# Kernel tuning notes

Measured on AMD Instinct MI355X. Metric: run time of the kernel, lower is better.

## Reference

```python
import jax, jax.numpy as jnp
import numpy as np

NCLASSES = 21
CONF_THRESH = 0.5
IOU_THRESH = 0.45
TOP_K = 200
NMS_MAX_OUT = 400
NEG = jnp.float32(-1e9)  # sentinel for suppressed / below-threshold scores

B, N_BOXES = 8, 8732
LAST = NCLASSES + 4 * (NCLASSES - 1) + 1  # 102


def setup_inputs() -> dict:
    key = jax.random.key(0)
    kc, kxy, kwh, ke = jax.random.split(key, 4)
    conf = jax.random.uniform(kc, (B, N_BOXES, NCLASSES), dtype=jnp.float32)
    # plausible normalized boxes: xmin,ymin in [0,0.8], width/height in [0.01,0.2]
    xy = jax.random.uniform(kxy, (B, N_BOXES, NCLASSES - 1, 2), minval=0.0, maxval=0.8)
    wh = jax.random.uniform(kwh, (B, N_BOXES, NCLASSES - 1, 2), minval=0.01, maxval=0.2)
    boxes = jnp.concatenate([xy, xy + wh], axis=-1).reshape(B, N_BOXES, 4 * (NCLASSES - 1))
    extra = jax.random.uniform(ke, (B, N_BOXES, 1), dtype=jnp.float32)
    y_pred = jnp.concatenate([conf, boxes, extra], axis=-1)  # [B, N, 102]
    return {"y_pred": y_pred}


def _iou_one_vs_all(box, boxes):
    # box: [4] (xmin,ymin,xmax,ymax); boxes: [N,4]
    x1 = jnp.maximum(box[0], boxes[:, 0])
    y1 = jnp.maximum(box[1], boxes[:, 1])
    x2 = jnp.minimum(box[2], boxes[:, 2])
    y2 = jnp.minimum(box[3], boxes[:, 3])
    inter = jnp.maximum(x2 - x1, 0.0) * jnp.maximum(y2 - y1, 0.0)
    area_a = (box[2] - box[0]) * (box[3] - box[1])
    area_b = (boxes[:, 2] - boxes[:, 0]) * (boxes[:, 3] - boxes[:, 1])
    union = area_a + area_b - inter
    return jnp.where(union > 0.0, inter / union, 0.0)


def _nms_one_class(rows):
    # rows: [N, 7] = (class_id, conf, xmin, ymin, xmax, ymax, extra)
    n = rows.shape[0]
    scores0 = jnp.where(rows[:, 1] > CONF_THRESH, rows[:, 1], NEG)
    boxes = rows[:, 2:6]
    idx_range = jnp.arange(n)

    def step(live, _):
        best = jnp.argmax(live)
        valid = live[best] > NEG * 0.5  # any real score passed the threshold
        ious = _iou_one_vs_all(boxes[best], boxes)
        suppress = valid & ((ious > IOU_THRESH) | (idx_range == best))
        live = jnp.where(suppress, NEG, live)
        return live, (best, valid)

    _, (sel, selv) = jax.lax.scan(step, scores0, None, length=NMS_MAX_OUT)
    # gather selected rows; zero-pad invalid slots (matches tf.pad with 0)
    out = jnp.where(selv[:, None], rows[sel], 0.0)  # [NMS_MAX_OUT, 7]
    return out


def _per_image(item):
    # item: [N, 102]
    n = item.shape[0]
    conf = item[:, 1:NCLASSES]                                  # [N, C-1]
    boxes = item[:, NCLASSES:NCLASSES + 4 * (NCLASSES - 1)].reshape(n, NCLASSES - 1, 4)
    extra = item[:, -1]                                         # [N]
    class_ids = jnp.arange(1, NCLASSES, dtype=item.dtype)       # [C-1]
    rows = jnp.concatenate([
        jnp.broadcast_to(class_ids[:, None, None], (NCLASSES - 1, n, 1)),
        conf.T[:, :, None],
        jnp.transpose(boxes, (1, 0, 2)),
        jnp.broadcast_to(extra[None, :, None], (NCLASSES - 1, n, 1)),
    ], axis=-1)                                                 # [C-1, N, 7]
    per_class = jax.vmap(_nms_one_class)(rows)                  # [C-1, MAX_OUT, 7]
    filtered = per_class.reshape(-1, 7)                         # [(C-1)*MAX_OUT, 7]
    _, top_idx = jax.lax.top_k(filtered[:, 1], TOP_K)           # sorted descending
    return filtered[top_idx]                                    # [TOP_K, 7]


def reference(y_pred):
    return jax.vmap(_per_image)(y_pred)  # [B, TOP_K, 7]
```

## Files before the change

### kernel.cpp

```cpp
#include <hip/hip_runtime.h>
#include <cstdint>

#define NB 8
#define NBOX 8732
#define NCL 21
#define NCM1 20
#define LASTD 102
#define CONF_TH 0.5f
#define IOU_TH 0.45f
#define TOPK 200
#define MAXOUT 400
#define SELCAP 200
#define EMITN 256
#define NTASK (NB * NCM1)
#define THREADS 1024
#define NW 16
#define NIT 9
#define NBIN 2048
#define KPAD 8768
#define NBATCH (KPAD / 64)

#define MIDD ((double)IOU_TH + 0x1p-26)

struct SM {
    float4 selbox[SELCAP];
    float selA[SELCAP];
    uint64_t selkey[SELCAP];
    uint64_t keys[KPAD];
    uint64_t smask[2][64];
    unsigned long long supW[2][NW];
    int hist[NBIN];
    int binstart[NBIN];
    int wavetot[NW];
    int Mshare, nselshare, prevNshare, doneflag;
};

__device__ __forceinline__ int iou_sup(float4 a, float aA, float4 b, float bA) {
    float x1 = fmaxf(a.x, b.x), y1 = fmaxf(a.y, b.y);
    float x2 = fminf(a.z, b.z), y2 = fminf(a.w, b.w);
    float iw = fmaxf(__fsub_rn(x2, x1), 0.0f);
    float ih = fmaxf(__fsub_rn(y2, y1), 0.0f);
    float inter = __fmul_rn(iw, ih);
    float uni = __fsub_rn(__fadd_rn(aA, bA), inter);
    return (double)inter > MIDD * (double)uni;
}

__device__ __forceinline__ float4 load_box(const float* __restrict__ img,
                                           int boxoff, uint64_t key) {
    if ((key >> 32) == 0) return make_float4(0.f, 0.f, 0.f, 0.f);
    uint32_t i = 0xFFFFFFFFu - (uint32_t)key;
    const float* bp = img + (size_t)i * LASTD + boxoff;
    return make_float4(bp[0], bp[1], bp[2], bp[3]);
}

__device__ __forceinline__ float box_area(float4 b) {
    return __fmul_rn(__fsub_rn(b.z, b.x), __fsub_rn(b.w, b.y));
}

__global__ __launch_bounds__(THREADS) void nms_per_class(const float* __restrict__ yp,
                                                         float* __restrict__ rows) {
    __shared__ SM sm;
    const int task = blockIdx.x;
    const int b = task / NCM1;
    const int cm1 = task % NCM1;
    const int tid = threadIdx.x;
    const int lane = tid & 63;
    const int wav = tid >> 6;
    const float* img = yp + (size_t)b * NBOX * LASTD;
    const int boxoff = NCL + 4 * cm1;

    float confs[NIT];
    #pragma unroll
    for (int it = 0; it < NIT; ++it) {
        int idx = it * THREADS + tid;
        confs[it] = (idx < NBOX) ? img[(size_t)idx * LASTD + (1 + cm1)] : 0.0f;
    }
    sm.hist[tid] = 0; sm.hist[tid + THREADS] = 0;
    __syncthreads();

    #pragma unroll
    for (int it = 0; it < NIT; ++it) {
        int idx = it * THREADS + tid;
        if (idx < NBOX && confs[it] > CONF_TH) {
            int bin = (int)((__float_as_uint(confs[it]) - 0x3F000000u) >> 12);
            atomicAdd(&sm.hist[bin], 1);
        }
    }
    __syncthreads();

    int h0 = sm.hist[2 * tid], h1 = sm.hist[2 * tid + 1];
    int x = h0 + h1;
    int s = x;
    #pragma unroll
    for (int d = 1; d <= 32; d <<= 1) {
        int y = __shfl_down(s, d);
        if (lane + d < 64) s += y;
    }
    if (lane == 0) sm.wavetot[wav] = s;
    __syncthreads();
    int cross = 0;
    #pragma unroll
    for (int w = 0; w < NW; ++w)
        if (w > wav) cross += sm.wavetot[w];
    int Safter = cross + s - x;
    sm.binstart[2 * tid + 1] = Safter;
    sm.binstart[2 * tid] = Safter + h1;
    if (tid == 0) sm.Mshare = cross + s;
    sm.hist[2 * tid] = 0; sm.hist[2 * tid + 1] = 0;
    __syncthreads();

    #pragma unroll
    for (int it = 0; it < NIT; ++it) {
        int idx = it * THREADS + tid;
        if (idx < NBOX && confs[it] > CONF_TH) {
            uint32_t bits = __float_as_uint(confs[it]);
            int bin = (int)((bits - 0x3F000000u) >> 12);
            int slot = sm.binstart[bin] + atomicAdd(&sm.hist[bin], 1);
            sm.keys[slot] = ((uint64_t)bits << 32) |
                            (uint32_t)(0xFFFFFFFFu - (uint32_t)idx);
        }
    }
    __syncthreads();
    const int M = sm.Mshare;
    for (int m = M + tid; m < KPAD; m += THREADS) sm.keys[m] = 0;
    for (int f = tid; f < NBIN; f += THREADS) {
        int s0 = sm.binstart[f], h = sm.hist[f];
        for (int i2 = 1; i2 < h; ++i2) {
            uint64_t key = sm.keys[s0 + i2];
            int j = i2 - 1;
            while (j >= 0 && sm.keys[s0 + j] < key) {
                sm.keys[s0 + j + 1] = sm.keys[s0 + j];
                --j;
            }
            sm.keys[s0 + j + 1] = key;
        }
    }
    __syncthreads();

    uint64_t keyC = sm.keys[lane];
    uint64_t keyN = sm.keys[64 + lane];
    float4 boxC = load_box(img, boxoff, keyC);
    float4 boxN = load_box(img, boxoff, keyN);
    float aC = box_area(boxC), aN = box_area(boxN);
    #pragma unroll
    for (int tt = 0; tt < 4; ++tt) {
        int c = wav + tt * NW;
        float4 cb;
        cb.x = __shfl(boxC.x, c); cb.y = __shfl(boxC.y, c);
        cb.z = __shfl(boxC.z, c); cb.w = __shfl(boxC.w, c);
        float ca = __shfl(aC, c);
        uint64_t row = 0;
        if (ca > 0.0f)
            row = __ballot(lane < c && iou_sup(cb, ca, boxC, aC));
        if (lane == 0) sm.smask[0][c] = row;
    }
    if (tid < 2 * NW) ((unsigned long long*)sm.supW)[tid] = 0ull;
    __syncthreads();

    int nsel = 0, prevN = 0;
    bool done = false;
    for (int i = 0; i < NBATCH && !done; ++i) {
        const int p = i & 1;
        const bool vC = (keyC >> 32) != 0;
        {
            int sup = 0;
            for (int j = prevN + wav; j < nsel; j += NW)
                sup |= iou_sup(boxC, aC, sm.selbox[j], sm.selA[j]);
            unsigned long long bal = __ballot(vC && sup);
            if (lane == 0 && bal) atomicOr(&sm.supW[p][wav], bal);
        }
        int f0 = (i + 2) * 64;
        uint64_t key2 = (f0 < KPAD) ? sm.keys[f0 + lane] : 0;
        float4 box2 = load_box(img, boxoff, key2);
        float a2 = box_area(box2);
        __syncthreads();
        const int nselPre = nsel;
        if (wav == 0) {
            unsigned long long V = __ballot(vC);
            unsigned long long E = (lane < NW) ? sm.supW[p][lane] : 0ull;
            #pragma unroll
            for (int d = 1; d < NW; d <<= 1) E |= __shfl_xor(E, d);
            E = __shfl(E, 0);
            if (lane < NW) sm.supW[p][lane] = 0ull;
            uint64_t smc = sm.smask[p][lane];
            uint64_t alive = ~(E | ~V);
            uint64_t accm = 0;
            int cnt = nsel;
            while (alive && cnt < SELCAP) {
                int t = __ffsll((unsigned long long)alive) - 1;
                uint64_t bit = 1ull << t;
                accm |= bit;
                cnt++;
                unsigned long long kill = __ballot((smc >> t) & 1ull);
                alive &= ~(kill | bit);
            }
            if ((accm >> lane) & 1ull) {
                int pos = nsel + __popcll(accm & ((1ull << lane) - 1ull));
                sm.selbox[pos] = boxC;
                sm.selA[pos] = aC;
                sm.selkey[pos] = keyC;
            }
            if (lane == 0) {
                sm.nselshare = cnt;
                sm.prevNshare = nsel;
                sm.doneflag = (cnt >= SELCAP) || (V != ~0ull);
            }
        } else {
            float4 cb[5];
            float ca[5];
            unsigned amask = 0;
            #pragma unroll
            for (int k = 0; k < 5; ++k) {
                int c = (wav - 1) + k * (NW - 1);
                float4 t4 = make_float4(0.f, 0.f, 0.f, 0.f);
                float tA = 0.0f;
                if (c < 64) {
                    t4.x = __shfl(boxN.x, c); t4.y = __shfl(boxN.y, c);
                    t4.z = __shfl(boxN.z, c); t4.w = __shfl(boxN.w, c);
                    tA = __shfl(aN, c);
                }
                cb[k] = t4; ca[k] = tA;
                if (c < 64 && tA > 0.0f) amask |= 1u << k;
            }
            unsigned long long sb = 0;
            for (int j0 = 0; j0 < nselPre && amask; j0 += 64) {
                int j = j0 + lane;
                bool jv = j < nselPre;
                float4 sbx = sm.selbox[jv ? j : 0];
                float sA = sm.selA[jv ? j : 0];
                #pragma unroll
                for (int k = 0; k < 5; ++k) {
                    if (!((amask >> k) & 1u)) continue;
                    int hit = jv && iou_sup(cb[k], ca[k], sbx, sA);
                    if (__ballot(hit)) {
                        amask &= ~(1u << k);
                        sb |= 1ull << ((wav - 1) + k * (NW - 1));
                    }
                }
            }
            #pragma unroll
            for (int k = 0; k < 5; ++k) {
                if (!((amask >> k) & 1u)) continue;
                int c = (wav - 1) + k * (NW - 1);
                uint64_t row = __ballot(lane < c && iou_sup(cb[k], ca[k], boxN, aN));
                if (lane == 0) sm.smask[p ^ 1][c] = row;
            }
            if (lane == 0) sm.supW[p ^ 1][wav] = sb;
        }
        __syncthreads();
        nsel = sm.nselshare;
        prevN = sm.prevNshare;
        done = sm.doneflag != 0;
        keyC = keyN; boxC = boxN; aC = aN;
        keyN = key2; boxN = box2; aN = a2;
    }

    float* out0 = rows + (size_t)task * MAXOUT * 7;
    for (int r = tid; r < EMITN; r += THREADS) {
        float* o = out0 + (size_t)r * 7;
        if (r < nsel) {
            uint64_t key = sm.selkey[r];
            uint32_t i = 0xFFFFFFFFu - (uint32_t)key;
            float4 bx = sm.selbox[r];
            o[0] = (float)(cm1 + 1);
            o[1] = __uint_as_float((uint32_t)(key >> 32));
            o[2] = bx.x;
            o[3] = bx.y;
            o[4] = bx.z;
            o[5] = bx.w;
            o[6] = img[(size_t)i * LASTD + (LASTD - 1)];
        } else {
            #pragma unroll
            for (int q = 0; q < 7; ++q) o[q] = 0.0f;
        }
    }
}

__global__ __launch_bounds__(THREADS) void topk_per_image(const float* __restrict__ rows,
                                                          float* __restrict__ out) {
    __shared__ uint64_t K[8192];
    const int b = blockIdx.x;
    const int tid = threadIdx.x;
    const float* rb = rows + (size_t)b * (NCM1 * MAXOUT) * 7;

    for (int xx = tid; xx < 8192; xx += THREADS) {
        int list = xx >> 8, r = xx & 255;
        uint64_t k = 0;
        if (list < NCM1) {
            int flat = list * MAXOUT + r;
            float conf = rb[(size_t)flat * 7 + 1];
            k = ((uint64_t)__float_as_uint(conf) << 32) |
                (uint32_t)(0xFFFFFFFFu - (uint32_t)flat);
        }
        K[xx] = k;
    }
    __syncthreads();

    for (int round = 0; round < 5; ++round) {
        int npairs = 16 >> round;
        int sep = 256 << round;
        for (int w = tid; w < npairs * 256; w += THREADS) {
            int p = w >> 8, t = w & 255;
            int A = p * 2 * sep;
            uint64_t a = K[A + t];
            uint64_t c = K[A + sep + 255 - t];
            K[A + t] = a > c ? a : c;
        }
        __syncthreads();
        for (int j = 128; j >= 1; j >>= 1) {
            for (int w = tid; w < npairs * 128; w += THREADS) {
                int p = w >> 7, q = w & 127;
                int t = ((q & ~(j - 1)) << 1) | (q & (j - 1));
                int A = p * 2 * sep;
                uint64_t x0 = K[A + t];
                uint64_t x1 = K[A + t + j];
                if (x0 < x1) { K[A + t] = x1; K[A + t + j] = x0; }
            }
            __syncthreads();
        }
    }

    if (tid < TOPK) {
        uint64_t key = K[tid];
        uint32_t flat = 0xFFFFFFFFu - (uint32_t)key;
        const float* src = rb + (size_t)flat * 7;
        float* o = out + ((size_t)b * TOPK + tid) * 7;
        #pragma unroll
        for (int q = 0; q < 7; ++q) o[q] = src[q];
    }
}

extern "C" void kernel_launch(void* const* d_in, const int* in_sizes, int n_in,
                              void* d_out, int out_size, void* d_ws, size_t ws_size,
                              hipStream_t stream) {
    const float* yp = (const float*)d_in[0];
    float* rows = (float*)d_ws;
    float* out = (float*)d_out;

    hipLaunchKernelGGL(nms_per_class, dim3(NTASK), dim3(THREADS), 0, stream, yp, rows);
    hipLaunchKernelGGL(topk_per_image, dim3(NB), dim3(THREADS), 0, stream, rows, out);
}
```

Measured before the change: 67.57 us.

## Split per-class NMS into key-building and greedy-scan kernels via global workspace

```diff
diff --git a/kernel.cpp b/kernel.cpp
--- a/kernel.cpp
+++ b/kernel.cpp
@@ -57,18 +57,15 @@
     return __fmul_rn(__fsub_rn(b.z, b.x), __fsub_rn(b.w, b.y));
 }
 
-__global__ __launch_bounds__(THREADS) void nms_per_class(const float* __restrict__ yp,
-                                                         float* __restrict__ rows) {
-    __shared__ SM sm;
-    const int task = blockIdx.x;
-    const int b = task / NCM1;
-    const int cm1 = task % NCM1;
-    const int tid = threadIdx.x;
-    const int lane = tid & 63;
-    const int wav = tid >> 6;
-    const float* img = yp + (size_t)b * NBOX * LASTD;
-    const int boxoff = NCL + 4 * cm1;
-
+__device__ __forceinline__ float4 shfl_box(float4 b, int c) {
+    float4 r;
+    r.x = __shfl(b.x, c); r.y = __shfl(b.y, c);
+    r.z = __shfl(b.z, c); r.w = __shfl(b.w, c);
+    return r;
+}
+
+__device__ void build_keys(const float* __restrict__ img, int cm1, SM& sm,
+                           int tid, int lane, int wav) {
     float confs[NIT];
     #pragma unroll
     for (int it = 0; it < NIT; ++it) {
@@ -136,7 +133,10 @@
         }
     }
     __syncthreads();
-
+}
+
+__device__ int greedy_scan(const float* __restrict__ img, int boxoff, SM& sm,
+                           int tid, int lane, int wav) {
     uint64_t keyC = sm.keys[lane];
     uint64_t keyN = sm.keys[64 + lane];
     float4 boxC = load_box(img, boxoff, keyC);
@@ -145,9 +145,7 @@
     #pragma unroll
     for (int tt = 0; tt < 4; ++tt) {
         int c = wav + tt * NW;
-        float4 cb;
-        cb.x = __shfl(boxC.x, c); cb.y = __shfl(boxC.y, c);
-        cb.z = __shfl(boxC.z, c); cb.w = __shfl(boxC.w, c);
+        float4 cb = shfl_box(boxC, c);
         float ca = __shfl(aC, c);
         uint64_t row = 0;
         if (ca > 0.0f)
@@ -215,8 +213,7 @@
                 float4 t4 = make_float4(0.f, 0.f, 0.f, 0.f);
                 float tA = 0.0f;
                 if (c < 64) {
-                    t4.x = __shfl(boxN.x, c); t4.y = __shfl(boxN.y, c);
-                    t4.z = __shfl(boxN.z, c); t4.w = __shfl(boxN.w, c);
+                    t4 = shfl_box(boxN, c);
                     tA = __shfl(aN, c);
                 }
                 cb[k] = t4; ca[k] = tA;
@@ -254,7 +251,12 @@
         keyC = keyN; boxC = boxN; aC = aN;
         keyN = key2; boxN = box2; aN = a2;
     }
-
+    return nsel;
+}
+
+__device__ void emit_rows(const float* __restrict__ img, int cm1, SM& sm,
+                          int nsel, float* __restrict__ rows, int task,
+                          int tid) {
     float* out0 = rows + (size_t)task * MAXOUT * 7;
     for (int r = tid; r < EMITN; r += THREADS) {
         float* o = out0 + (size_t)r * 7;
@@ -276,6 +278,48 @@
     }
 }
 
+__global__ __launch_bounds__(THREADS) void nms_front(const float* __restrict__ yp,
+                                                     uint64_t* __restrict__ keysG) {
+    __shared__ SM sm;
+    const int task = blockIdx.x;
+    const int b = task / NCM1;
+    const int cm1 = task % NCM1;
+    const int tid = threadIdx.x;
+    const float* img = yp + (size_t)b * NBOX * LASTD;
+    build_keys(img, cm1, sm, tid, tid & 63, tid >> 6);
+    uint64_t* kg = keysG + (size_t)task * KPAD;
+    for (int m = tid; m < KPAD; m += THREADS) kg[m] = sm.keys[m];
+}
+
+__global__ __launch_bounds__(THREADS) void nms_scan(const float* __restrict__ yp,
+                                                    const uint64_t* __restrict__ keysG,
+                                                    float* __restrict__ rows) {
+    __shared__ SM sm;
+    const int task = blockIdx.x;
+    const int b = task / NCM1;
+    const int cm1 = task % NCM1;
+    const int tid = threadIdx.x;
+    const float* img = yp + (size_t)b * NBOX * LASTD;
+    const uint64_t* kg = keysG + (size_t)task * KPAD;
+    for (int m = tid; m < KPAD; m += THREADS) sm.keys[m] = kg[m];
+    __syncthreads();
+    int nsel = greedy_scan(img, NCL + 4 * cm1, sm, tid, tid & 63, tid >> 6);
+    emit_rows(img, cm1, sm, nsel, rows, task, tid);
+}
+
+__global__ __launch_bounds__(THREADS) void nms_mono(const float* __restrict__ yp,
+                                                    float* __restrict__ rows) {
+    __shared__ SM sm;
+    const int task = blockIdx.x;
+    const int b = task / NCM1;
+    const int cm1 = task % NCM1;
+    const int tid = threadIdx.x;
+    const float* img = yp + (size_t)b * NBOX * LASTD;
+    build_keys(img, cm1, sm, tid, tid & 63, tid >> 6);
+    int nsel = greedy_scan(img, NCL + 4 * cm1, sm, tid, tid & 63, tid >> 6);
+    emit_rows(img, cm1, sm, nsel, rows, task, tid);
+}
+
 __global__ __launch_bounds__(THREADS) void topk_per_image(const float* __restrict__ rows,
                                                           float* __restrict__ out) {
     __shared__ uint64_t K[8192];
@@ -335,8 +379,20 @@
                               hipStream_t stream) {
     const float* yp = (const float*)d_in[0];
     float* rows = (float*)d_ws;
+    const size_t rowsB = (size_t)NTASK * MAXOUT * 7 * sizeof(float);
+    uint64_t* keysG = (uint64_t*)((char*)d_ws + rowsB);
+    const size_t need = rowsB + (size_t)NTASK * KPAD * sizeof(uint64_t);
     float* out = (float*)d_out;
 
-    hipLaunchKernelGGL(nms_per_class, dim3(NTASK), dim3(THREADS), 0, stream, yp, rows);
-    hipLaunchKernelGGL(topk_per_image, dim3(NB), dim3(THREADS), 0, stream, rows, out);
-}
+    if (ws_size >= need) {
+        hipLaunchKernelGGL(nms_front, dim3(NTASK), dim3(THREADS), 0, stream,
+                           yp, keysG);
+        hipLaunchKernelGGL(nms_scan, dim3(NTASK), dim3(THREADS), 0, stream,
+                           yp, keysG, rows);
+    } else {
+        hipLaunchKernelGGL(nms_mono, dim3(NTASK), dim3(THREADS), 0, stream,
+                           yp, rows);
+    }
+    hipLaunchKernelGGL(topk_per_image, dim3(NB), dim3(THREADS), 0, stream,
+                       rows, out);
+}
```

Result: slower. 75.45 us (+11.7%).
